# Optimization experiments

Measured on AMD Instinct MI355X. Metric: run time of the kernel, lower is better.

The kernel has to match this reference:

```python
import math
import jax, jax.numpy as jnp
import numpy as np

B, T, C = 2, 2048, 1024
NH = 16
HS = C // NH
WIN = 256

def setup_inputs() -> dict:
    key = jax.random.key(0)
    k1, k2, k3 = jax.random.split(key, 3)
    x = jax.random.normal(k1, (B, T, C), dtype=jnp.float32)
    # Linear weights stored as (in, out) so y = x @ W
    scale_attn = 1.0 / math.sqrt(C)
    W_attn = jax.random.normal(k2, (C, 3 * C), dtype=jnp.float32) * scale_attn
    W_proj = jax.random.normal(k3, (C, C), dtype=jnp.float32) * scale_attn
    return {"x": x, "W_attn": W_attn, "W_proj": W_proj}

def reference(x, W_attn, W_proj):
    Bs, Ts, Cs = x.shape
    W = min(WIN, Ts)
    qkv = x @ W_attn                                  # [B,T,3C]
    q, k, v = jnp.split(qkv, 3, axis=-1)
    # [B,T,C] -> [B,NH,T,HS]
    q = q.reshape(Bs, Ts, NH, HS).transpose(0, 2, 1, 3)
    k = k.reshape(Bs, Ts, NH, HS).transpose(0, 2, 1, 3)
    v = v.reshape(Bs, Ts, NH, HS).transpose(0, 2, 1, 3)
    att = jnp.einsum('bhqd,bhkd->bhqk', q, k) * (1.0 / math.sqrt(HS))
    i_idx = jnp.arange(Ts)[:, None]
    j_idx = jnp.arange(Ts)[None, :]
    mask = (j_idx <= i_idx) & (i_idx - j_idx < W)      # causal sliding window
    att = jnp.where(mask[None, None, :, :], att, -jnp.inf)
    att = jax.nn.softmax(att, axis=-1)
    y = jnp.einsum('bhqk,bhkd->bhqd', att, v)          # [B,NH,T,HS]
    y = y.transpose(0, 2, 1, 3).reshape(Bs, Ts, Cs)
    return y @ W_proj
```

## Files before the change

kernel.cpp:

```cpp
#include <hip/hip_runtime.h>
#include <hip/hip_bf16.h>
#include <cstdint>

#define B_   2
#define T_   2048
#define C_   1024
#define NH_  16
#define HS_  64
#define WIN_ 256
#define M_   (B_*T_)

typedef __attribute__((ext_vector_type(8)))  short          short8;
typedef __attribute__((ext_vector_type(8)))  unsigned short ushortx8;
typedef __attribute__((ext_vector_type(8)))  __bf16         bf16x8;
typedef __attribute__((ext_vector_type(4)))  float          floatx4;
typedef __attribute__((ext_vector_type(16))) float          floatx16;

__device__ __forceinline__ unsigned short f2bf(float f) {
    union { float f; uint32_t u; } v; v.f = f;
    uint32_t r = (v.u + 0x7FFFu + ((v.u >> 16) & 1u)) >> 16;
    return (unsigned short)r;
}

__device__ __forceinline__ floatx4 mfma16(short8 a, short8 b, floatx4 c) {
    return __builtin_amdgcn_mfma_f32_16x16x32_bf16(
        __builtin_bit_cast(bf16x8, a), __builtin_bit_cast(bf16x8, b), c, 0, 0, 0);
}
__device__ __forceinline__ floatx16 mfma32(short8 a, short8 b, floatx16 c) {
    return __builtin_amdgcn_mfma_f32_32x32x16_bf16(
        __builtin_bit_cast(bf16x8, a), __builtin_bit_cast(bf16x8, b), c, 0, 0, 0);
}

__device__ __forceinline__ void async16(const void* g, void* l) {
    __builtin_amdgcn_global_load_lds(
        (const __attribute__((address_space(1))) void*)g,
        (__attribute__((address_space(3))) void*)l, 16, 0, 0);
}

#define NB_CONV 4096
#define NB_WA   768
#define NB_WP   256

__device__ void transpose_tile(const float* __restrict__ in, unsigned short* __restrict__ out,
                               int K, int N, int kt, int nt, unsigned short (*tile)[65])
{
    const int k0 = kt * 64, n0 = nt * 64;
    const int tr = threadIdx.x >> 4;
    const int tc = (threadIdx.x & 15) * 4;
    #pragma unroll
    for (int it = 0; it < 4; it++) {
        int row = tr + it * 16;
        float4 v = *(const float4*)&in[(size_t)(k0 + row) * N + n0 + tc];
        tile[row][tc + 0] = f2bf(v.x);
        tile[row][tc + 1] = f2bf(v.y);
        tile[row][tc + 2] = f2bf(v.z);
        tile[row][tc + 3] = f2bf(v.w);
    }
    __syncthreads();
    #pragma unroll
    for (int it = 0; it < 4; it++) {
        int nrow = tr + it * 16;
        ushort4 h;
        h.x = tile[tc + 0][nrow]; h.y = tile[tc + 1][nrow];
        h.z = tile[tc + 2][nrow]; h.w = tile[tc + 3][nrow];
        *(ushort4*)&out[(size_t)(n0 + nrow) * K + k0 + tc] = h;
    }
}

__global__ __launch_bounds__(256)
void prep_kernel(const float* __restrict__ x, const float* __restrict__ W_attn,
                 const float* __restrict__ W_proj,
                 unsigned short* __restrict__ xb, unsigned short* __restrict__ Wa_t,
                 unsigned short* __restrict__ Wp_t)
{
    __shared__ unsigned short tile[64][65];
    const int bid = blockIdx.x;
    if (bid < NB_CONV) {
        int i = (bid * 256 + threadIdx.x) * 4;
        float4 v = *(const float4*)&x[i];
        ushort4 h;
        h.x = f2bf(v.x); h.y = f2bf(v.y); h.z = f2bf(v.z); h.w = f2bf(v.w);
        *(ushort4*)&xb[i] = h;
    } else if (bid < NB_CONV + NB_WA) {
        int idx = bid - NB_CONV;
        transpose_tile(W_attn, Wa_t, C_, 3 * C_, idx / 48, idx % 48, tile);
    } else {
        int idx = bid - NB_CONV - NB_WA;
        transpose_tile(W_proj, Wp_t, C_, C_, idx / 16, idx % 16, tile);
    }
}

template<int MT, bool OUT_BF16, bool VSPLIT>
__global__ __launch_bounds__(256)
void gemm32(const unsigned short* __restrict__ A,
            const unsigned short* __restrict__ Bt,
            void* __restrict__ Cp, unsigned short* __restrict__ vt,
            int M, int N, int K)
{
    constexpr int BK = 64;
    constexpr int BM = 64 * MT;
    __shared__ unsigned short As[BM * BK];
    __shared__ unsigned short Bs[128 * BK];

    const int tid  = threadIdx.x;
    const int lane = tid & 63;
    const int wave = tid >> 6;
    const int l32  = lane & 31;
    const int hi   = lane >> 5;
    const int px   = l32 & 7;
    const int wm   = (wave & 1) * 32 * MT;
    const int wn   = (wave >> 1) * 64;
    const int m0   = blockIdx.y * BM;
    const int n0   = blockIdx.x * 128;

    const int ri = lane >> 3;
    const int pg = lane & 7;
    const int gg = pg ^ ri;

    floatx16 acc[MT][2];
    #pragma unroll
    for (int i = 0; i < MT; i++)
        #pragma unroll
        for (int j = 0; j < 2; j++) acc[i][j] = (floatx16)(0.f);

    const unsigned short* gA = &A[(size_t)(m0 + wave * 8 + ri) * K + gg * 8];
    const unsigned short* gB = &Bt[(size_t)(n0 + wave * 8 + ri) * K + gg * 8];
    unsigned short* lA = &As[(wave * 8) * BK];
    unsigned short* lB = &Bs[(wave * 8) * BK];

    for (int k0 = 0; k0 < K; k0 += BK) {
        #pragma unroll
        for (int s = 0; s < 2 * MT; s++)
            async16(gA + k0 + (size_t)s * 32 * K, lA + s * 32 * BK);
        #pragma unroll
        for (int s = 0; s < 4; s++)
            async16(gB + k0 + (size_t)s * 32 * K, lB + s * 32 * BK);
        __syncthreads();

        #pragma unroll
        for (int ks = 0; ks < 4; ks++) {
            short8 af[MT], bfr[2];
            #pragma unroll
            for (int i = 0; i < MT; i++) {
                int r = wm + i * 32 + l32;
                int p = (ks * 2 + hi) ^ px;
                af[i] = *(const short8*)(&As[r * BK + p * 8]);
            }
            #pragma unroll
            for (int j = 0; j < 2; j++) {
                int r = wn + j * 32 + l32;
                int p = (ks * 2 + hi) ^ px;
                bfr[j] = *(const short8*)(&Bs[r * BK + p * 8]);
            }
            #pragma unroll
            for (int i = 0; i < MT; i++)
                #pragma unroll
                for (int j = 0; j < 2; j++)
                    acc[i][j] = mfma32(af[i], bfr[j], acc[i][j]);
        }
        __syncthreads();
    }

    #pragma unroll
    for (int i = 0; i < MT; i++)
        #pragma unroll
        for (int j = 0; j < 2; j++) {
            const int col  = n0 + wn + j * 32 + l32;
            const int row0 = m0 + wm + i * 32 + 4 * hi;
            if (VSPLIT && col >= 2 * C_) {
                const int hd = col - 2 * C_;
                const int hh = hd >> 6, d = hd & 63;
                #pragma unroll
                for (int g = 0; g < 4; g++) {
                    int rowg = row0 + 8 * g;
                    int bb = rowg >> 11, t = rowg & (T_ - 1);
                    ushort4 h4;
                    h4.x = f2bf(acc[i][j][g * 4 + 0]);
                    h4.y = f2bf(acc[i][j][g * 4 + 1]);
                    h4.z = f2bf(acc[i][j][g * 4 + 2]);
                    h4.w = f2bf(acc[i][j][g * 4 + 3]);
                    *(ushort4*)&vt[((size_t)(bb * NH_ + hh) * 64 + d) * T_ + t] = h4;
                }
            } else {
                #pragma unroll
                for (int g = 0; g < 4; g++)
                    #pragma unroll
                    for (int rr = 0; rr < 4; rr++) {
                        int row = row0 + 8 * g + rr;
                        if (OUT_BF16)
                            ((unsigned short*)Cp)[(size_t)row * N + col] = f2bf(acc[i][j][g * 4 + rr]);
                        else
                            ((float*)Cp)[(size_t)row * N + col] = acc[i][j][g * 4 + rr];
                    }
            }
        }
}

__global__ __launch_bounds__(256)
void attn_kernel(const unsigned short* __restrict__ qkv,
                 const unsigned short* __restrict__ vt,
                 unsigned short* __restrict__ y)
{
    __shared__ unsigned short Ks[64 * 64];
    __shared__ unsigned short Vs[64 * 64];
    __shared__ unsigned short Ps[4][16 * 72];

    const int tid  = threadIdx.x;
    const int lane = tid & 63;
    const int wave = tid >> 6;
    const int l16  = lane & 15;
    const int quad = lane >> 4;
    const int sw   = l16 & 7;

    const int g  = blockIdx.x;
    const int yq = g >> 3;
    const int hb = (g & 7) + 8 * (yq >> 5);
    const int qt = yq & 31;
    const int h  = hb & 15;
    const int b  = hb >> 4;

    const int q0b = qt * 64;
    const int q0w = q0b + wave * 16;
    const size_t base = (size_t)b * T_;
    const int ROW  = 3 * C_;
    const int qoff = h * HS_;
    const int koff = C_ + h * HS_;
    const size_t vbase = ((size_t)(b * NH_ + h) * 64) * T_;
    unsigned short* Pstrip = Ps[wave];
    const float SC = 0.125f * 1.44269504f;

    const int ri = lane >> 3;
    const int gg = (lane & 7) ^ ri;

    short8 aq[2];
    #pragma unroll
    for (int ks = 0; ks < 2; ks++)
        aq[ks] = *(const short8*)&qkv[(base + q0w + l16) * ROW + qoff + ks * 32 + quad * 8];

    floatx4 O[4];
    #pragma unroll
    for (int j = 0; j < 4; j++) O[j] = (floatx4){0.f, 0.f, 0.f, 0.f};
    float psum[4] = {0.f, 0.f, 0.f, 0.f};

    int kb_lo = q0b - (WIN_ - 1);
    kb_lo = (kb_lo > 0 ? kb_lo : 0) & ~63;

    for (int kb = kb_lo; kb <= q0b; kb += 64) {
        __syncthreads();
        #pragma unroll
        for (int c = 0; c < 2; c++) {
            int row = wave * 16 + c * 8;
            async16(&qkv[(base + kb + row + ri) * ROW + koff + gg * 8],
                    &Ks[row * 64]);
            async16(&vt[vbase + (size_t)(row + ri) * T_ + kb + gg * 8],
                    &Vs[row * 64]);
        }
        __syncthreads();

        floatx4 s[4];
        #pragma unroll
        for (int nt = 0; nt < 4; nt++) s[nt] = (floatx4){0.f, 0.f, 0.f, 0.f};
        #pragma unroll
        for (int ks = 0; ks < 2; ks++)
            #pragma unroll
            for (int nt = 0; nt < 4; nt++) {
                short8 bk = *(const short8*)&Ks[(nt * 16 + l16) * 64
                                                + (((ks * 4 + quad) ^ sw) * 8)];
                s[nt] = mfma16(aq[ks], bk, s[nt]);
            }

        #pragma unroll
        for (int nt = 0; nt < 4; nt++)
            #pragma unroll
            for (int r = 0; r < 4; r++) {
                int dist = (q0w + quad * 4 + r) - (kb + nt * 16 + l16);
                float sv = ((unsigned)dist < (unsigned)WIN_) ? s[nt][r] * SC : -1e30f;
                float e = exp2f(sv);
                psum[r] += e;
                s[nt][r] = e;
            }

        #pragma unroll
        for (int nt = 0; nt < 4; nt++)
            #pragma unroll
            for (int r = 0; r < 4; r++)
                Pstrip[(quad * 4 + r) * 72 + nt * 16 + l16] = f2bf(s[nt][r]);

        #pragma unroll
        for (int ks = 0; ks < 2; ks++) {
            short8 ap = *(const short8*)&Pstrip[l16 * 72 + ks * 32 + quad * 8];
            #pragma unroll
            for (int jt = 0; jt < 4; jt++) {
                short8 bv = *(const short8*)&Vs[(jt * 16 + l16) * 64
                                                + (((ks * 4 + quad) ^ sw) * 8)];
                O[jt] = mfma16(ap, bv, O[jt]);
            }
        }
    }

    #pragma unroll
    for (int r = 0; r < 4; r++) {
        #pragma unroll
        for (int off = 8; off >= 1; off >>= 1)
            psum[r] += __shfl_xor(psum[r], off, 64);
    }

    #pragma unroll
    for (int jt = 0; jt < 4; jt++)
        #pragma unroll
        for (int r = 0; r < 4; r++)
            Pstrip[(quad * 4 + r) * 72 + jt * 16 + l16] = f2bf(O[jt][r] / psum[r]);
    #pragma unroll
    for (int it = 0; it < 2; it++) {
        int c = lane + 64 * it;
        int qr = c >> 3, dc = (c & 7) * 8;
        *(ushortx8*)&y[(base + q0w + qr) * C_ + qoff + dc] =
            *(const ushortx8*)&Pstrip[qr * 72 + dc];
    }
}

extern "C" void kernel_launch(void* const* d_in, const int* in_sizes, int n_in,
                              void* d_out, int out_size, void* d_ws, size_t ws_size,
                              hipStream_t stream)
{
    const float* x      = (const float*)d_in[0];
    const float* W_attn = (const float*)d_in[1];
    const float* W_proj = (const float*)d_in[2];
    float* out = (float*)d_out;

    unsigned short* xb   = (unsigned short*)d_ws;
    unsigned short* Wa_t = xb   + (size_t)M_ * C_;
    unsigned short* Wp_t = Wa_t + (size_t)3 * C_ * C_;
    unsigned short* qkv  = Wp_t + (size_t)C_ * C_;
    unsigned short* y    = qkv  + (size_t)M_ * 3 * C_;
    unsigned short* vtg  = y    + (size_t)M_ * C_;

    dim3 blk(256);
    prep_kernel<<<NB_CONV + NB_WA + NB_WP, blk, 0, stream>>>(x, W_attn, W_proj, xb, Wa_t, Wp_t);
    gemm32<2, true, true><<<dim3((3 * C_) / 128, M_ / 128), blk, 0, stream>>>(
        xb, Wa_t, qkv, vtg, M_, 3 * C_, C_);
    attn_kernel<<<(T_ / 64) * NH_ * B_, blk, 0, stream>>>(qkv, vtg, y);
    gemm32<1, false, false><<<dim3(C_ / 128, M_ / 64), blk, 0, stream>>>(
        y, Wp_t, out, nullptr, M_, C_, C_);
}
```

Before: 152.3 us.

## Process 128 query rows per attention block with double-buffered K/V tiles

Each attention block now covers 128 query rows instead of 64, with each wave owning two 16-row strips. Every K/V tile loaded into LDS is therefore reused by twice as many queries, which halves the global K/V traffic per query. The K/V shared buffers are double-buffered so the next tile's async load is issued before the current tile is computed. Strips skip tiles outside their causal window. The cost is fewer blocks in the grid, more registers per wave for the doubled accumulators, and extra loop iterations in which only some strips do work.

```diff
diff --git a/kernel.cpp b/kernel.cpp
--- a/kernel.cpp
+++ b/kernel.cpp
@@ -201,8 +201,8 @@
                  const unsigned short* __restrict__ vt,
                  unsigned short* __restrict__ y)
 {
-    __shared__ unsigned short Ks[64 * 64];
-    __shared__ unsigned short Vs[64 * 64];
+    __shared__ unsigned short Ks[2][64 * 64];
+    __shared__ unsigned short Vs[2][64 * 64];
     __shared__ unsigned short Ps[4][16 * 72];
 
     const int tid  = threadIdx.x;
@@ -214,13 +214,12 @@
 
     const int g  = blockIdx.x;
     const int yq = g >> 3;
-    const int hb = (g & 7) + 8 * (yq >> 5);
-    const int qt = yq & 31;
+    const int qt = yq & 15;
+    const int hb = (g & 7) + 8 * (yq >> 4);
     const int h  = hb & 15;
     const int b  = hb >> 4;
 
-    const int q0b = qt * 64;
-    const int q0w = q0b + wave * 16;
+    const int q0b = qt * 128;
     const size_t base = (size_t)b * T_;
     const int ROW  = 3 * C_;
     const int qoff = h * HS_;
@@ -232,90 +231,117 @@
     const int ri = lane >> 3;
     const int gg = (lane & 7) ^ ri;
 
-    short8 aq[2];
-    #pragma unroll
-    for (int ks = 0; ks < 2; ks++)
-        aq[ks] = *(const short8*)&qkv[(base + q0w + l16) * ROW + qoff + ks * 32 + quad * 8];
-
-    floatx4 O[4];
-    #pragma unroll
-    for (int j = 0; j < 4; j++) O[j] = (floatx4){0.f, 0.f, 0.f, 0.f};
-    float psum[4] = {0.f, 0.f, 0.f, 0.f};
+    const int sq0 = q0b + (wave * 2 + 0) * 16;
+    const int sq1 = q0b + (wave * 2 + 1) * 16;
+
+    short8 aq[2][2];
+    #pragma unroll
+    for (int ks = 0; ks < 2; ks++) {
+        aq[0][ks] = *(const short8*)&qkv[(base + sq0 + l16) * ROW + qoff + ks * 32 + quad * 8];
+        aq[1][ks] = *(const short8*)&qkv[(base + sq1 + l16) * ROW + qoff + ks * 32 + quad * 8];
+    }
+
+    floatx4 O[2][4];
+    #pragma unroll
+    for (int hf = 0; hf < 2; hf++)
+        #pragma unroll
+        for (int j = 0; j < 4; j++) O[hf][j] = (floatx4){0.f, 0.f, 0.f, 0.f};
+    float psum[2][4] = {{0.f,0.f,0.f,0.f},{0.f,0.f,0.f,0.f}};
 
     int kb_lo = q0b - (WIN_ - 1);
     kb_lo = (kb_lo > 0 ? kb_lo : 0) & ~63;
-
-    for (int kb = kb_lo; kb <= q0b; kb += 64) {
+    const int kb_hi = q0b + 64;
+
+    #pragma unroll
+    for (int c = 0; c < 2; c++) {
+        int row = wave * 16 + c * 8;
+        async16(&qkv[(base + kb_lo + row + ri) * ROW + koff + gg * 8], &Ks[0][row * 64]);
+        async16(&vt[vbase + (size_t)(row + ri) * T_ + kb_lo + gg * 8],  &Vs[0][row * 64]);
+    }
+
+    int p = 0;
+    for (int kb = kb_lo; kb <= kb_hi; kb += 64, p ^= 1) {
         __syncthreads();
-        #pragma unroll
-        for (int c = 0; c < 2; c++) {
-            int row = wave * 16 + c * 8;
-            async16(&qkv[(base + kb + row + ri) * ROW + koff + gg * 8],
-                    &Ks[row * 64]);
-            async16(&vt[vbase + (size_t)(row + ri) * T_ + kb + gg * 8],
-                    &Vs[row * 64]);
-        }
-        __syncthreads();
-
-        floatx4 s[4];
-        #pragma unroll
-        for (int nt = 0; nt < 4; nt++) s[nt] = (floatx4){0.f, 0.f, 0.f, 0.f};
-        #pragma unroll
-        for (int ks = 0; ks < 2; ks++)
-            #pragma unroll
-            for (int nt = 0; nt < 4; nt++) {
-                short8 bk = *(const short8*)&Ks[(nt * 16 + l16) * 64
-                                                + (((ks * 4 + quad) ^ sw) * 8)];
-                s[nt] = mfma16(aq[ks], bk, s[nt]);
-            }
-
-        #pragma unroll
-        for (int nt = 0; nt < 4; nt++)
-            #pragma unroll
-            for (int r = 0; r < 4; r++) {
-                int dist = (q0w + quad * 4 + r) - (kb + nt * 16 + l16);
-                float sv = ((unsigned)dist < (unsigned)WIN_) ? s[nt][r] * SC : -1e30f;
-                float e = exp2f(sv);
-                psum[r] += e;
-                s[nt][r] = e;
-            }
-
-        #pragma unroll
-        for (int nt = 0; nt < 4; nt++)
+        if (kb + 64 <= kb_hi) {
+            #pragma unroll
+            for (int c = 0; c < 2; c++) {
+                int row = wave * 16 + c * 8;
+                async16(&qkv[(base + kb + 64 + row + ri) * ROW + koff + gg * 8],
+                        &Ks[p ^ 1][row * 64]);
+                async16(&vt[vbase + (size_t)(row + ri) * T_ + kb + 64 + gg * 8],
+                        &Vs[p ^ 1][row * 64]);
+            }
+        }
+
+        #pragma unroll
+        for (int hf = 0; hf < 2; hf++) {
+            const int q0w = (hf == 0) ? sq0 : sq1;
+            if (kb > q0w + 15) continue;
+            if (kb + 63 < q0w - (WIN_ - 1)) continue;
+
+            floatx4 s[4];
+            #pragma unroll
+            for (int nt = 0; nt < 4; nt++) s[nt] = (floatx4){0.f, 0.f, 0.f, 0.f};
+            #pragma unroll
+            for (int ks = 0; ks < 2; ks++)
+                #pragma unroll
+                for (int nt = 0; nt < 4; nt++) {
+                    short8 bk = *(const short8*)&Ks[p][(nt * 16 + l16) * 64
+                                                      + (((ks * 4 + quad) ^ sw) * 8)];
+                    s[nt] = mfma16(aq[hf][ks], bk, s[nt]);
+                }
+
+            #pragma unroll
+            for (int nt = 0; nt < 4; nt++)
+                #pragma unroll
+                for (int r = 0; r < 4; r++) {
+                    int dist = (q0w + quad * 4 + r) - (kb + nt * 16 + l16);
+                    float sv = ((unsigned)dist < (unsigned)WIN_) ? s[nt][r] * SC : -1e30f;
+                    float e = exp2f(sv);
+                    psum[hf][r] += e;
+                    s[nt][r] = e;
+                }
+
+            #pragma unroll
+            for (int nt = 0; nt < 4; nt++)
+                #pragma unroll
+                for (int r = 0; r < 4; r++)
+                    Pstrip[(quad * 4 + r) * 72 + nt * 16 + l16] = f2bf(s[nt][r]);
+
+            #pragma unroll
+            for (int ks = 0; ks < 2; ks++) {
+                short8 ap = *(const short8*)&Pstrip[l16 * 72 + ks * 32 + quad * 8];
+                #pragma unroll
+                for (int jt = 0; jt < 4; jt++) {
+                    short8 bv = *(const short8*)&Vs[p][(jt * 16 + l16) * 64
+                                                      + (((ks * 4 + quad) ^ sw) * 8)];
+                    O[hf][jt] = mfma16(ap, bv, O[hf][jt]);
+                }
+            }
+        }
+    }
+
+    #pragma unroll
+    for (int hf = 0; hf < 2; hf++) {
+        const int q0w = (hf == 0) ? sq0 : sq1;
+        #pragma unroll
+        for (int r = 0; r < 4; r++) {
+            #pragma unroll
+            for (int off = 8; off >= 1; off >>= 1)
+                psum[hf][r] += __shfl_xor(psum[hf][r], off, 64);
+        }
+        #pragma unroll
+        for (int jt = 0; jt < 4; jt++)
             #pragma unroll
             for (int r = 0; r < 4; r++)
-                Pstrip[(quad * 4 + r) * 72 + nt * 16 + l16] = f2bf(s[nt][r]);
-
-        #pragma unroll
-        for (int ks = 0; ks < 2; ks++) {
-            short8 ap = *(const short8*)&Pstrip[l16 * 72 + ks * 32 + quad * 8];
-            #pragma unroll
-            for (int jt = 0; jt < 4; jt++) {
-                short8 bv = *(const short8*)&Vs[(jt * 16 + l16) * 64
-                                                + (((ks * 4 + quad) ^ sw) * 8)];
-                O[jt] = mfma16(ap, bv, O[jt]);
-            }
-        }
-    }
-
-    #pragma unroll
-    for (int r = 0; r < 4; r++) {
-        #pragma unroll
-        for (int off = 8; off >= 1; off >>= 1)
-            psum[r] += __shfl_xor(psum[r], off, 64);
-    }
-
-    #pragma unroll
-    for (int jt = 0; jt < 4; jt++)
-        #pragma unroll
-        for (int r = 0; r < 4; r++)
-            Pstrip[(quad * 4 + r) * 72 + jt * 16 + l16] = f2bf(O[jt][r] / psum[r]);
-    #pragma unroll
-    for (int it = 0; it < 2; it++) {
-        int c = lane + 64 * it;
-        int qr = c >> 3, dc = (c & 7) * 8;
-        *(ushortx8*)&y[(base + q0w + qr) * C_ + qoff + dc] =
-            *(const ushortx8*)&Pstrip[qr * 72 + dc];
+                Pstrip[(quad * 4 + r) * 72 + jt * 16 + l16] = f2bf(O[hf][jt][r] / psum[hf][r]);
+        #pragma unroll
+        for (int it = 0; it < 2; it++) {
+            int c = lane + 64 * it;
+            int qr = c >> 3, dc = (c & 7) * 8;
+            *(ushortx8*)&y[(base + q0w + qr) * C_ + qoff + dc] =
+                *(const ushortx8*)&Pstrip[qr * 72 + dc];
+        }
     }
 }
 
@@ -339,7 +365,7 @@
     prep_kernel<<<NB_CONV + NB_WA + NB_WP, blk, 0, stream>>>(x, W_attn, W_proj, xb, Wa_t, Wp_t);
     gemm32<2, true, true><<<dim3((3 * C_) / 128, M_ / 128), blk, 0, stream>>>(
         xb, Wa_t, qkv, vtg, M_, 3 * C_, C_);
-    attn_kernel<<<(T_ / 64) * NH_ * B_, blk, 0, stream>>>(qkv, vtg, y);
+    attn_kernel<<<(T_ / 128) * NH_ * B_, blk, 0, stream>>>(qkv, vtg, y);
     gemm32<1, false, false><<<dim3(C_ / 128, M_ / 64), blk, 0, stream>>>(
         y, Wp_t, out, nullptr, M_, C_, C_);
 }
```

New measurement: 156.9 us. 1.03x slower.
